# Kernel optimization log

Measured on AMD Instinct MI355X. Metric: run time of the kernel, lower is better.

## Reference

```python
import jax, jax.numpy as jnp
import numpy as np


def setup_inputs() -> dict:
    key = jax.random.key(0)
    k1, k2, k3 = jax.random.split(key, 3)
    B, M, T, D = 512, 4096, 48, 2
    preds = jax.random.normal(k1, (B, M), dtype=jnp.float32)
    target = jax.random.normal(k2, (B, 1, T, D), dtype=jnp.float32)
    memory = jax.random.normal(k3, (M, T, D), dtype=jnp.float32)
    return {"preds": preds, "target": target, "memory": memory}


def reference(preds, target, memory):
    # preds: [B, M]; target: [B, 1, T, D]; memory: [M, T, D]
    gt = target[:, 0]                                  # [B, T, D]
    diff = memory[None, :, :, :] - gt[:, None, :, :]   # [B, M, T, D]
    # mean over timesteps of per-timestep euclidean distance
    dist = jnp.sqrt(jnp.sum(diff * diff, axis=-1)).mean(axis=-1)  # [B, M]
    true_index = jnp.argmin(dist, axis=1)              # [B] int labels
    # cross-entropy of preds vs. nearest-mode labels, averaged over batch
    logp = jax.nn.log_softmax(preds, axis=1)           # [B, M]
    nll = -jnp.take_along_axis(logp, true_index[:, None], axis=1)[:, 0]  # [B]
    loss = nll.mean()
    return loss, true_index.astype(jnp.float32)
```

## Files before the change

kernel.cpp:

```cpp
#include <hip/hip_runtime.h>
#include <math.h>

#define B 512
#define M 4096
#define T 48
#define MCHUNK 4
#define NCH (M / MCHUNK)


__global__ __launch_bounds__(256) void k_prep(const float* __restrict__ target,
                                              float4* __restrict__ tgtP,
                                              float* __restrict__ out0) {
    int i = blockIdx.x * 256 + threadIdx.x;
    if (i == 0) out0[0] = 0.0f;
    int b = i / (T / 2), q = i - b * (T / 2);
    float4 v = *(const float4*)(target + (size_t)b * (T * 2) + 4 * q);
    tgtP[q * B + b] = v;
}

__global__ __launch_bounds__(256, 8) void k_dist(const float4* __restrict__ tgtP,
                                                 const float* __restrict__ memory,
                                                 unsigned long long* __restrict__ pval) {
    const int tid = threadIdx.x;
    const int ch  = blockIdx.x;
    const int b   = blockIdx.y * 256 + tid;
    const int m0  = ch * MCHUNK;

    __shared__ float4 smem[MCHUNK * (T / 2)];
    if (tid < MCHUNK * (T / 2))
        smem[tid] = ((const float4*)(memory + (size_t)m0 * (T * 2)))[tid];
    __syncthreads();

    float acc0 = 0.f, acc1 = 0.f, acc2 = 0.f, acc3 = 0.f;

#pragma unroll 6
    for (int q = 0; q < T / 2; ++q) {
        float4 g = tgtP[q * B + b];
        {
            float4 mv = smem[0 * (T / 2) + q];
            float dx0 = mv.x - g.x, dy0 = mv.y - g.y;
            float dx1 = mv.z - g.z, dy1 = mv.w - g.w;
            acc0 += __builtin_amdgcn_sqrtf(fmaf(dx0, dx0, dy0 * dy0));
            acc0 += __builtin_amdgcn_sqrtf(fmaf(dx1, dx1, dy1 * dy1));
        }
        {
            float4 mv = smem[1 * (T / 2) + q];
            float dx0 = mv.x - g.x, dy0 = mv.y - g.y;
            float dx1 = mv.z - g.z, dy1 = mv.w - g.w;
            acc1 += __builtin_amdgcn_sqrtf(fmaf(dx0, dx0, dy0 * dy0));
            acc1 += __builtin_amdgcn_sqrtf(fmaf(dx1, dx1, dy1 * dy1));
        }
        {
            float4 mv = smem[2 * (T / 2) + q];
            float dx0 = mv.x - g.x, dy0 = mv.y - g.y;
            float dx1 = mv.z - g.z, dy1 = mv.w - g.w;
            acc2 += __builtin_amdgcn_sqrtf(fmaf(dx0, dx0, dy0 * dy0));
            acc2 += __builtin_amdgcn_sqrtf(fmaf(dx1, dx1, dy1 * dy1));
        }
        {
            float4 mv = smem[3 * (T / 2) + q];
            float dx0 = mv.x - g.x, dy0 = mv.y - g.y;
            float dx1 = mv.z - g.z, dy1 = mv.w - g.w;
            acc3 += __builtin_amdgcn_sqrtf(fmaf(dx0, dx0, dy0 * dy0));
            acc3 += __builtin_amdgcn_sqrtf(fmaf(dx1, dx1, dy1 * dy1));
        }
    }

    float bestv = acc0; int besti = m0;
    if (acc1 < bestv) { bestv = acc1; besti = m0 + 1; }
    if (acc2 < bestv) { bestv = acc2; besti = m0 + 2; }
    if (acc3 < bestv) { bestv = acc3; besti = m0 + 3; }

    pval[(size_t)b * NCH + ch] =
        ((unsigned long long)__float_as_uint(bestv) << 32) | (unsigned int)besti;
}

__global__ __launch_bounds__(256) void k_post(const float* __restrict__ preds,
                                              const unsigned long long* __restrict__ pval,
                                              float* __restrict__ out) {
    const int lane = threadIdx.x & 63;
    const int wv   = threadIdx.x >> 6;
    const int b    = blockIdx.x * 4 + wv;

    unsigned long long best = 0xFFFFFFFFFFFFFFFFULL;
#pragma unroll
    for (int j = 0; j < NCH / 64; ++j) {
        unsigned long long p = pval[(size_t)b * NCH + j * 64 + lane];
        if (p < best) best = p;
    }
#pragma unroll
    for (int s = 32; s > 0; s >>= 1) {
        unsigned long long o = __shfl_down(best, s);
        if (o < best) best = o;
    }
    best = __shfl(best, 0);
    const int idx = (int)(unsigned int)(best & 0xFFFFFFFFULL);

    const float4* row = (const float4*)(preds + (size_t)b * M);
    float4 v[16];
    float mx = -INFINITY;
#pragma unroll
    for (int j = 0; j < 16; ++j) {
        v[j] = row[j * 64 + lane];
        mx = fmaxf(mx, fmaxf(fmaxf(v[j].x, v[j].y), fmaxf(v[j].z, v[j].w)));
    }
#pragma unroll
    for (int s = 32; s > 0; s >>= 1) mx = fmaxf(mx, __shfl_down(mx, s));
    mx = __shfl(mx, 0);

    float sum = 0.f;
#pragma unroll
    for (int j = 0; j < 16; ++j)
        sum += expf(v[j].x - mx) + expf(v[j].y - mx) + expf(v[j].z - mx) + expf(v[j].w - mx);
#pragma unroll
    for (int s = 32; s > 0; s >>= 1) sum += __shfl_down(sum, s);

    if (lane == 0) {
        float lse = mx + logf(sum);
        float nll = lse - preds[(size_t)b * M + idx];
        atomicAdd(out, nll * (1.0f / B));
        out[1 + b] = (float)idx;
    }
}

extern "C" void kernel_launch(void* const* d_in, const int* in_sizes, int n_in,
                              void* d_out, int out_size, void* d_ws, size_t ws_size,
                              hipStream_t stream) {
    const float* preds  = (const float*)d_in[0];
    const float* target = (const float*)d_in[1];
    const float* memory = (const float*)d_in[2];
    float* out = (float*)d_out;

    char* ws = (char*)d_ws;
    unsigned long long* pval = (unsigned long long*)ws;
    float4* tgtP = (float4*)(ws + (size_t)4 * 1024 * 1024);

    k_prep<<<(B * T / 2) / 256, 256, 0, stream>>>(target, tgtP, out);
    dim3 g1(NCH, B / 256);
    k_dist<<<g1, 256, 0, stream>>>(tgtP, memory, pval);
    k_post<<<B / 4, 256, 0, stream>>>(preds, pval, out);
}
```

Measured before the change: 47.11 us.

## Split timesteps across waves and widen mode chunk with LDS reduction

Distance kernel now processes 8 memory modes per block and 128 batch rows, with each wave handling a slice of timesteps for two rows and reducing partial sums through shared memory before the per-chunk argmin. This raises reuse of target and memory values in registers and halves the number of per-chunk partial results written and later scanned. It adds shared-memory reduction, extra barriers and a lower occupancy bound.

```diff
diff --git a/kernel.cpp b/kernel.cpp
--- a/kernel.cpp
+++ b/kernel.cpp
@@ -1,11 +1,15 @@
 #include <hip/hip_runtime.h>
 #include <math.h>
+
+typedef unsigned long long u64;
 
 #define B 512
 #define M 4096
 #define T 48
-#define MCHUNK 4
+#define MCHUNK 8
 #define NCH (M / MCHUNK)
+#define BGRP 128
+#define QW 6
 
 
 __global__ __launch_bounds__(256) void k_prep(const float* __restrict__ target,
@@ -18,79 +22,95 @@
     tgtP[q * B + b] = v;
 }
 
-__global__ __launch_bounds__(256, 8) void k_dist(const float4* __restrict__ tgtP,
+__global__ __launch_bounds__(256, 4) void k_dist(const float4* __restrict__ tgtP,
                                                  const float* __restrict__ memory,
-                                                 unsigned long long* __restrict__ pval) {
-    const int tid = threadIdx.x;
-    const int ch  = blockIdx.x;
-    const int b   = blockIdx.y * 256 + tid;
-    const int m0  = ch * MCHUNK;
+                                                 u64* __restrict__ pval) {
+    const int tid  = threadIdx.x;
+    const int lane = tid & 63;
+    const int w    = tid >> 6;
+    const int ch   = blockIdx.x;
+    const int m0   = ch * MCHUNK;
+    const int b0   = blockIdx.y * BGRP;
 
     __shared__ float4 smem[MCHUNK * (T / 2)];
+    __shared__ float  part[4][MCHUNK][BGRP];
+    __shared__ float  sum[MCHUNK][BGRP];
+
     if (tid < MCHUNK * (T / 2))
-        smem[tid] = ((const float4*)(memory + (size_t)m0 * (T * 2)))[tid];
+        smem[tid] = ((const float4*)memory)[(size_t)m0 * (T / 2) + tid];
+
+    float4 ga[QW], gb[QW];
+#pragma unroll
+    for (int j = 0; j < QW; ++j) {
+        ga[j] = tgtP[(QW * w + j) * B + b0 + lane];
+        gb[j] = tgtP[(QW * w + j) * B + b0 + 64 + lane];
+    }
     __syncthreads();
 
-    float acc0 = 0.f, acc1 = 0.f, acc2 = 0.f, acc3 = 0.f;
+    float acc0[MCHUNK], acc1[MCHUNK];
+#pragma unroll
+    for (int mi = 0; mi < MCHUNK; ++mi) { acc0[mi] = 0.f; acc1[mi] = 0.f; }
 
-#pragma unroll 6
-    for (int q = 0; q < T / 2; ++q) {
-        float4 g = tgtP[q * B + b];
-        {
-            float4 mv = smem[0 * (T / 2) + q];
-            float dx0 = mv.x - g.x, dy0 = mv.y - g.y;
-            float dx1 = mv.z - g.z, dy1 = mv.w - g.w;
-            acc0 += __builtin_amdgcn_sqrtf(fmaf(dx0, dx0, dy0 * dy0));
-            acc0 += __builtin_amdgcn_sqrtf(fmaf(dx1, dx1, dy1 * dy1));
-        }
-        {
-            float4 mv = smem[1 * (T / 2) + q];
-            float dx0 = mv.x - g.x, dy0 = mv.y - g.y;
-            float dx1 = mv.z - g.z, dy1 = mv.w - g.w;
-            acc1 += __builtin_amdgcn_sqrtf(fmaf(dx0, dx0, dy0 * dy0));
-            acc1 += __builtin_amdgcn_sqrtf(fmaf(dx1, dx1, dy1 * dy1));
-        }
-        {
-            float4 mv = smem[2 * (T / 2) + q];
-            float dx0 = mv.x - g.x, dy0 = mv.y - g.y;
-            float dx1 = mv.z - g.z, dy1 = mv.w - g.w;
-            acc2 += __builtin_amdgcn_sqrtf(fmaf(dx0, dx0, dy0 * dy0));
-            acc2 += __builtin_amdgcn_sqrtf(fmaf(dx1, dx1, dy1 * dy1));
-        }
-        {
-            float4 mv = smem[3 * (T / 2) + q];
-            float dx0 = mv.x - g.x, dy0 = mv.y - g.y;
-            float dx1 = mv.z - g.z, dy1 = mv.w - g.w;
-            acc3 += __builtin_amdgcn_sqrtf(fmaf(dx0, dx0, dy0 * dy0));
-            acc3 += __builtin_amdgcn_sqrtf(fmaf(dx1, dx1, dy1 * dy1));
+#pragma unroll
+    for (int j = 0; j < QW; ++j) {
+        const float4 g0 = ga[j], g1 = gb[j];
+#pragma unroll
+        for (int mi = 0; mi < MCHUNK; ++mi) {
+            float4 mv = smem[mi * (T / 2) + QW * w + j];
+            float dx, dy;
+            dx = mv.x - g0.x; dy = mv.y - g0.y;
+            acc0[mi] += __builtin_amdgcn_sqrtf(fmaf(dx, dx, dy * dy));
+            dx = mv.z - g0.z; dy = mv.w - g0.w;
+            acc0[mi] += __builtin_amdgcn_sqrtf(fmaf(dx, dx, dy * dy));
+            dx = mv.x - g1.x; dy = mv.y - g1.y;
+            acc1[mi] += __builtin_amdgcn_sqrtf(fmaf(dx, dx, dy * dy));
+            dx = mv.z - g1.z; dy = mv.w - g1.w;
+            acc1[mi] += __builtin_amdgcn_sqrtf(fmaf(dx, dx, dy * dy));
         }
     }
 
-    float bestv = acc0; int besti = m0;
-    if (acc1 < bestv) { bestv = acc1; besti = m0 + 1; }
-    if (acc2 < bestv) { bestv = acc2; besti = m0 + 2; }
-    if (acc3 < bestv) { bestv = acc3; besti = m0 + 3; }
+#pragma unroll
+    for (int mi = 0; mi < MCHUNK; ++mi) {
+        part[w][mi][lane]      = acc0[mi];
+        part[w][mi][64 + lane] = acc1[mi];
+    }
+    __syncthreads();
 
-    pval[(size_t)b * NCH + ch] =
-        ((unsigned long long)__float_as_uint(bestv) << 32) | (unsigned int)besti;
+#pragma unroll
+    for (int k = 0; k < 4; ++k) {
+        int item = k * 256 + tid;
+        int mi = item >> 7, bb = item & (BGRP - 1);
+        sum[mi][bb] = part[0][mi][bb] + part[1][mi][bb]
+                    + part[2][mi][bb] + part[3][mi][bb];
+    }
+    __syncthreads();
+
+    if (tid < BGRP) {
+        float bv = sum[0][tid]; int bi = m0;
+#pragma unroll
+        for (int mi = 1; mi < MCHUNK; ++mi)
+            if (sum[mi][tid] < bv) { bv = sum[mi][tid]; bi = m0 + mi; }
+        pval[(size_t)(b0 + tid) * NCH + ch] =
+            ((u64)__float_as_uint(bv) << 32) | (unsigned int)bi;
+    }
 }
 
 __global__ __launch_bounds__(256) void k_post(const float* __restrict__ preds,
-                                              const unsigned long long* __restrict__ pval,
+                                              const u64* __restrict__ pval,
                                               float* __restrict__ out) {
     const int lane = threadIdx.x & 63;
     const int wv   = threadIdx.x >> 6;
     const int b    = blockIdx.x * 4 + wv;
 
-    unsigned long long best = 0xFFFFFFFFFFFFFFFFULL;
+    u64 best = 0xFFFFFFFFFFFFFFFFULL;
 #pragma unroll
     for (int j = 0; j < NCH / 64; ++j) {
-        unsigned long long p = pval[(size_t)b * NCH + j * 64 + lane];
+        u64 p = pval[(size_t)b * NCH + j * 64 + lane];
         if (p < best) best = p;
     }
 #pragma unroll
     for (int s = 32; s > 0; s >>= 1) {
-        unsigned long long o = __shfl_down(best, s);
+        u64 o = __shfl_down(best, s);
         if (o < best) best = o;
     }
     best = __shfl(best, 0);
@@ -132,11 +152,11 @@
     float* out = (float*)d_out;
 
     char* ws = (char*)d_ws;
-    unsigned long long* pval = (unsigned long long*)ws;
-    float4* tgtP = (float4*)(ws + (size_t)4 * 1024 * 1024);
+    u64* pval    = (u64*)ws;
+    float4* tgtP = (float4*)(ws + (size_t)2 * 1024 * 1024);
 
     k_prep<<<(B * T / 2) / 256, 256, 0, stream>>>(target, tgtP, out);
-    dim3 g1(NCH, B / 256);
+    dim3 g1(NCH, B / BGRP);
     k_dist<<<g1, 256, 0, stream>>>(tgtP, memory, pval);
     k_post<<<B / 4, 256, 0, stream>>>(preds, pval, out);
 }
```

New measurement: 44.61 us. -5.3%, faster.
